# Optimization experiments

Measured on AMD Instinct MI355X. Metric: run time of the kernel, lower is better.

The kernel has to match this reference:

```python
import jax, jax.numpy as jnp
import numpy as np

IN_DIM = 256
OUT_DIM = 256
NUM_HEADS = 4
HEAD_DIM = OUT_DIM // NUM_HEADS
N_SRC = 100000
N_DST = 50000
N_EDGES = 300000


def setup_inputs() -> dict:
    key = jax.random.key(0)
    ks = jax.random.split(key, 10)
    h_src = jax.random.normal(ks[0], (N_SRC, IN_DIM), dtype=jnp.float32)
    h_dst = jax.random.normal(ks[1], (N_DST, IN_DIM), dtype=jnp.float32)
    src_idx = jax.random.randint(ks[2], (N_EDGES,), 0, N_SRC)
    dst_idx = jax.random.randint(ks[3], (N_EDGES,), 0, N_DST)
    # torch nn.Linear weights are [out, in]; xavier-uniform init, zero bias
    def xavier(k, shape):
        limit = jnp.sqrt(6.0 / (shape[0] + shape[1]))
        return jax.random.uniform(k, shape, jnp.float32, -limit, limit)
    Wq = xavier(ks[4], (OUT_DIM, IN_DIM))
    Wk = xavier(ks[5], (OUT_DIM, IN_DIM))
    Wv = xavier(ks[6], (OUT_DIM, IN_DIM))
    bq = jnp.zeros((OUT_DIM,), jnp.float32)
    bk = jnp.zeros((OUT_DIM,), jnp.float32)
    bv = jnp.zeros((OUT_DIM,), jnp.float32)
    return {"h_src": h_src, "h_dst": h_dst, "src_idx": src_idx, "dst_idx": dst_idx,
            "Wq": Wq, "bq": bq, "Wk": Wk, "bk": bk, "Wv": Wv, "bv": bv}


def reference(h_src, h_dst, src_idx, dst_idx, Wq, bq, Wk, bk, Wv, bv):
    # Projections (torch Linear: x @ W.T + b), reshape to [N, H, Dh]
    Q = (h_dst @ Wq.T + bq).reshape(-1, NUM_HEADS, HEAD_DIM)
    K = (h_src @ Wk.T + bk).reshape(-1, NUM_HEADS, HEAD_DIM)
    V = (h_src @ Wv.T + bv).reshape(-1, NUM_HEADS, HEAD_DIM)

    # Edge scores: u_dot_v('K','Q') -> per-edge, per-head dot product [E, H]
    score = jnp.einsum('ehd,ehd->eh', K[src_idx], Q[dst_idx]) / jnp.sqrt(
        jnp.asarray(HEAD_DIM, jnp.float32))

    # Edge softmax grouped by destination (per head), numerically stable
    seg_max = jax.ops.segment_max(score, dst_idx, num_segments=N_DST)
    seg_max = jnp.where(jnp.isfinite(seg_max), seg_max, 0.0)
    e = jnp.exp(score - seg_max[dst_idx])
    seg_sum = jax.ops.segment_sum(e, dst_idx, num_segments=N_DST)
    a = e / seg_sum[dst_idx]  # [E, H]

    # Weighted sum aggregation: u_mul_e then sum per destination
    m = V[src_idx] * a[:, :, None]  # [E, H, Dh]
    h = jax.ops.segment_sum(m, dst_idx, num_segments=N_DST)  # [N_dst, H, Dh]
    return h.reshape(-1, OUT_DIM)
```

## Files before the change

### kernel.cpp

```cpp
#include <hip/hip_runtime.h>
#include <hip/hip_bf16.h>
#include <stdint.h>

#define IN_DIM    256
#define OUT_DIM   256
#define NUM_HEADS 4
#define HEAD_DIM  64
#define N_SRC     100000
#define N_DST     50000
#define N_EDGES   300000

#define BM 128
#define BN 256
#define BK 32
#define SCAN_NBLK ((N_DST + 1023) / 1024)

typedef __attribute__((ext_vector_type(8))) short v8s;
typedef __attribute__((ext_vector_type(4))) float v4f;

__device__ __forceinline__ unsigned short f2bf(float f) {
    unsigned u = __float_as_uint(f);
    unsigned r = (u + 0x7FFFu + ((u >> 16) & 1u)) >> 16;
    return (unsigned short)r;
}
__device__ __forceinline__ float bf2f(unsigned short s) {
    return __uint_as_float(((unsigned)s) << 16);
}

__device__ __forceinline__ void async_copy16(const unsigned short* g,
                                             unsigned short* l) {
    __builtin_amdgcn_global_load_lds(
        (const __attribute__((address_space(1))) unsigned int*)g,
        (__attribute__((address_space(3))) unsigned int*)l, 16, 0, 0);
}

__global__ void wcvt_kernel(const float* __restrict__ wq,
                            const float* __restrict__ wk,
                            const float* __restrict__ wv,
                            unsigned short* __restrict__ dst) {
    int i = blockIdx.x * 256 + threadIdx.x;
    if (i >= 3 * 8192) return;
    int m = i >> 13;
    int r = i & 8191;
    const float* s = (m == 0) ? wq : (m == 1) ? wk : wv;
    const float4* sp = (const float4*)(s + (size_t)r * 8);
    float4 x = sp[0], y = sp[1];
    v8s o;
    o[0] = (short)f2bf(x.x); o[1] = (short)f2bf(x.y);
    o[2] = (short)f2bf(x.z); o[3] = (short)f2bf(x.w);
    o[4] = (short)f2bf(y.x); o[5] = (short)f2bf(y.y);
    o[6] = (short)f2bf(y.z); o[7] = (short)f2bf(y.w);
    *(v8s*)(dst + (size_t)m * 65536 + (size_t)r * 8) = o;
}

__global__ __launch_bounds__(512, 2) void gemm_kernel(
    const float* __restrict__ h_src, const float* __restrict__ h_dst,
    const unsigned short* __restrict__ Wb,
    const float* __restrict__ bq, const float* __restrict__ bk,
    const float* __restrict__ bv,
    unsigned short* __restrict__ Q, unsigned short* __restrict__ K,
    unsigned short* __restrict__ V) {

    __shared__ unsigned short smem[24576];

    int z = blockIdx.z;
    const float* A; const unsigned short* W;
    const float* bias; unsigned short* Out; int M;
    if (z == 0)      { A = h_dst; W = Wb;          bias = bq; Out = Q; M = N_DST; }
    else if (z == 1) { A = h_src; W = Wb + 65536;  bias = bk; Out = K; M = N_SRC; }
    else             { A = h_src; W = Wb + 131072; bias = bv; Out = V; M = N_SRC; }

    int mbase = blockIdx.x * BM;
    if (mbase >= M) return;

    int tid  = threadIdx.x;
    int wave = tid >> 6, lane = tid & 63;
    int lm = lane & 15, quad = lane >> 4;
    int wrow = wave >> 2;
    int wcol = wave & 3;

    int ar = tid >> 2, akc = (tid & 3) * 8;
    int gr = mbase + ar; if (gr > M - 1) gr = M - 1;
    const float* gA = A + (size_t)gr * 256 + akc;

    int sr = lane >> 2, skc = (lane & 3) * 8;
    const unsigned short* gB0 = W + (size_t)(wave * 32 + sr) * 256 + skc;
    const unsigned short* gB1 = gB0 + (size_t)16 * 256;

    v4f acc[4][4];
#pragma unroll
    for (int i = 0; i < 4; i++)
#pragma unroll
        for (int j = 0; j < 4; j++) acc[i][j] = (v4f){0, 0, 0, 0};

    const int NK = 256 / BK;

    float4 xc, yc;
    {
        float4 x0 = *(const float4*)(gA);
        float4 y0 = *(const float4*)(gA + 4);
        async_copy16(gB0, &smem[8192 + (wave * 32) * 32]);
        async_copy16(gB1, &smem[8192 + (wave * 32 + 16) * 32]);
        xc = *(const float4*)(gA + BK);
        yc = *(const float4*)(gA + BK + 4);
        v8s o;
        o[0] = (short)f2bf(x0.x); o[1] = (short)f2bf(x0.y);
        o[2] = (short)f2bf(x0.z); o[3] = (short)f2bf(x0.w);
        o[4] = (short)f2bf(y0.x); o[5] = (short)f2bf(y0.y);
        o[6] = (short)f2bf(y0.z); o[7] = (short)f2bf(y0.w);
        *(v8s*)&smem[(size_t)ar * 32 + akc] = o;
        asm volatile("s_waitcnt vmcnt(2) lgkmcnt(0)" ::: "memory");
        __builtin_amdgcn_s_barrier();
        __builtin_amdgcn_sched_barrier(0);
    }

    int buf = 0;
#pragma unroll
    for (int ks = 0; ks < NK; ks++) {
        float4 xn, yn;
        if (ks + 1 < NK) {
            int k0 = (ks + 1) * BK;
            async_copy16(gB0 + k0,
                         &smem[8192 + (buf ^ 1) * 8192 + (wave * 32) * 32]);
            async_copy16(gB1 + k0,
                         &smem[8192 + (buf ^ 1) * 8192 + (wave * 32 + 16) * 32]);
        }
        if (ks + 2 < NK) {
            int k0 = (ks + 2) * BK;
            xn = *(const float4*)(gA + k0);
            yn = *(const float4*)(gA + k0 + 4);
        }

        const unsigned short* sAb = smem + buf * 4096;
        const unsigned short* sBb = smem + 8192 + buf * 8192;
        v8s af[4], bfr[4];
#pragma unroll
        for (int i = 0; i < 4; i++)
            af[i] = *(const v8s*)&sAb[(wrow * 64 + i * 16 + lm) * 32 + quad * 8];
#pragma unroll
        for (int j = 0; j < 4; j++)
            bfr[j] = *(const v8s*)&sBb[(wcol * 64 + j * 16 + lm) * 32 + quad * 8];
#pragma unroll
        for (int i = 0; i < 4; i++)
#pragma unroll
            for (int j = 0; j < 4; j++)
                acc[i][j] = __builtin_amdgcn_mfma_f32_16x16x32_bf16(
                    af[i], bfr[j], acc[i][j], 0, 0, 0);

        if (ks + 1 < NK) {
            v8s o;
            o[0] = (short)f2bf(xc.x); o[1] = (short)f2bf(xc.y);
            o[2] = (short)f2bf(xc.z); o[3] = (short)f2bf(xc.w);
            o[4] = (short)f2bf(yc.x); o[5] = (short)f2bf(yc.y);
            o[6] = (short)f2bf(yc.z); o[7] = (short)f2bf(yc.w);
            *(v8s*)&smem[(buf ^ 1) * 4096 + (size_t)ar * 32 + akc] = o;
            if (ks + 2 < NK)
                asm volatile("s_waitcnt vmcnt(2) lgkmcnt(0)" ::: "memory");
            else
                asm volatile("s_waitcnt vmcnt(0) lgkmcnt(0)" ::: "memory");
            __builtin_amdgcn_s_barrier();
            __builtin_amdgcn_sched_barrier(0);
        }
        xc = xn; yc = yn;
        buf ^= 1;
    }

#pragma unroll
    for (int p = 0; p < 2; p++) {
        __syncthreads();
        if (wrow == p) {
#pragma unroll
            for (int j = 0; j < 4; j++) {
                int col = wcol * 64 + j * 16 + lm;
                float bcol = bias[col];
#pragma unroll
                for (int i = 0; i < 4; i++)
#pragma unroll
                    for (int r = 0; r < 4; r++)
                        smem[(i * 16 + quad * 4 + r) * 256 + col] =
                            f2bf(acc[i][j][r] + bcol);
            }
        }
        __syncthreads();
#pragma unroll
        for (int k = 0; k < 4; k++) {
            int c = tid + k * 512;
            int rl = c >> 5, ch = c & 31;
            int grow = mbase + p * 64 + rl;
            if (grow < M)
                *(v8s*)(Out + (size_t)grow * 256 + ch * 8) =
                    *(const v8s*)&smem[rl * 256 + ch * 8];
        }
    }
}

__global__ void hist_kernel(const int* __restrict__ dst_idx,
                            int* __restrict__ cnt) {
    int i = blockIdx.x * 256 + threadIdx.x;
    if (i < N_EDGES) atomicAdd(&cnt[dst_idx[i]], 1);
}

__global__ __launch_bounds__(1024) void scan_local_kernel(
    const int* __restrict__ cnt, int* __restrict__ offsets,
    int* __restrict__ bsum) {
    __shared__ int wsum[16];
    int t = threadIdx.x, b = blockIdx.x;
    int i = b * 1024 + t;
    int lane = t & 63, w = t >> 6;
    int v = (i < N_DST) ? cnt[i] : 0;
    int s = v;
#pragma unroll
    for (int off = 1; off < 64; off <<= 1) {
        int u = __shfl_up(s, off, 64);
        if (lane >= off) s += u;
    }
    if (lane == 63) wsum[w] = s;
    __syncthreads();
    if (w == 0) {
        int x = (lane < 16) ? wsum[lane] : 0;
#pragma unroll
        for (int off = 1; off < 16; off <<= 1) {
            int u = __shfl_up(x, off, 64);
            if (lane >= off) x += u;
        }
        if (lane < 16) wsum[lane] = x;
    }
    __syncthreads();
    int wbase = (w == 0) ? 0 : wsum[w - 1];
    if (i < N_DST) offsets[i] = wbase + s - v;
    if (t == 1023) bsum[b] = wsum[15];
}

__global__ void scan_base_kernel(int* __restrict__ bsum,
                                 int* __restrict__ offsets) {
    int lane = threadIdx.x;
    int v = (lane < SCAN_NBLK) ? bsum[lane] : 0;
    int s = v;
#pragma unroll
    for (int off = 1; off < 64; off <<= 1) {
        int u = __shfl_up(s, off, 64);
        if (lane >= off) s += u;
    }
    if (lane < SCAN_NBLK) bsum[lane] = s - v;
    if (lane == 0) offsets[N_DST] = N_EDGES;
}

__global__ __launch_bounds__(1024) void scan_fixup_kernel(
    int* __restrict__ offsets, int* __restrict__ cursor,
    const int* __restrict__ bsum) {
    int i = blockIdx.x * 1024 + threadIdx.x;
    if (i >= N_DST) return;
    int off = offsets[i] + bsum[i >> 10];
    offsets[i] = off;
    cursor[i] = off;
}

__global__ void scatter_kernel(const int* __restrict__ src_idx,
                               const int* __restrict__ dst_idx,
                               int* __restrict__ cursor,
                               int* __restrict__ esrc) {
    int i = blockIdx.x * 256 + threadIdx.x;
    if (i >= N_EDGES) return;
    int d = dst_idx[i];
    int pos = atomicAdd(&cursor[d], 1);
    esrc[pos] = src_idx[i];
}

__global__ __launch_bounds__(256) void agg_kernel(
    const int* __restrict__ esrc, const int* __restrict__ offsets,
    const unsigned short* __restrict__ Q, const unsigned short* __restrict__ K,
    const unsigned short* __restrict__ V, float* __restrict__ out) {

    int wave = threadIdx.x >> 6, lane = threadIdx.x & 63;
    int d = blockIdx.x * 4 + wave;
    if (d >= N_DST) return;

    int start = offsets[d], end = offsets[d + 1];
    float4 o = make_float4(0.f, 0.f, 0.f, 0.f);

    if (end > start) {
        ushort4 qv = *((const ushort4*)(Q + (size_t)d * 256) + lane);
        float q0 = bf2f(qv.x), q1 = bf2f(qv.y), q2 = bf2f(qv.z), q3 = bf2f(qv.w);

        float m = -3.0e38f, l = 0.f;
        float a0 = 0.f, a1 = 0.f, a2 = 0.f, a3 = 0.f;

        int s0 = esrc[start];
        int sN = (start + 1 < end) ? esrc[start + 1] : 0;
        ushort4 kv = *((const ushort4*)(K + (size_t)s0 * 256) + lane);
        ushort4 vv = *((const ushort4*)(V + (size_t)s0 * 256) + lane);

        for (int j = start; j < end; j++) {
            ushort4 kc = kv, vc = vv;
            int sNN = (j + 2 < end) ? esrc[j + 2] : 0;
            if (j + 1 < end) {
                kv = *((const ushort4*)(K + (size_t)sN * 256) + lane);
                vv = *((const ushort4*)(V + (size_t)sN * 256) + lane);
            }
            sN = sNN;

            float p = bf2f(kc.x) * q0 + bf2f(kc.y) * q1 +
                      bf2f(kc.z) * q2 + bf2f(kc.w) * q3;
            p += __shfl_xor(p, 1, 64);
            p += __shfl_xor(p, 2, 64);
            p += __shfl_xor(p, 4, 64);
            p += __shfl_xor(p, 8, 64);
            p *= 0.125f;

            float mn = fmaxf(m, p);
            float sc = __expf(m - mn);
            float w  = __expf(p - mn);
            l = l * sc + w;
            a0 = a0 * sc + w * bf2f(vc.x);
            a1 = a1 * sc + w * bf2f(vc.y);
            a2 = a2 * sc + w * bf2f(vc.z);
            a3 = a3 * sc + w * bf2f(vc.w);
            m = mn;
        }
        float inv = 1.0f / l;
        o = make_float4(a0 * inv, a1 * inv, a2 * inv, a3 * inv);
    }
    *((float4*)(out + (size_t)d * 256) + lane) = o;
}

extern "C" void kernel_launch(void* const* d_in, const int* in_sizes, int n_in,
                              void* d_out, int out_size, void* d_ws, size_t ws_size,
                              hipStream_t stream) {
    const float* h_src   = (const float*)d_in[0];
    const float* h_dst   = (const float*)d_in[1];
    const int*   src_idx = (const int*)d_in[2];
    const int*   dst_idx = (const int*)d_in[3];
    const float* Wq      = (const float*)d_in[4];
    const float* bq      = (const float*)d_in[5];
    const float* Wk      = (const float*)d_in[6];
    const float* bk      = (const float*)d_in[7];
    const float* Wv      = (const float*)d_in[8];
    const float* bv      = (const float*)d_in[9];
    float* out = (float*)d_out;

    char* ws = (char*)d_ws;
    size_t off = 0;
    auto take = [&](size_t bytes) { char* p = ws + off; off = (off + bytes + 255) & ~(size_t)255; return p; };
    unsigned short* Q       = (unsigned short*)take((size_t)N_DST * 256 * 2);
    unsigned short* K       = (unsigned short*)take((size_t)N_SRC * 256 * 2);
    unsigned short* V       = (unsigned short*)take((size_t)N_SRC * 256 * 2);
    unsigned short* Wb      = (unsigned short*)take((size_t)3 * 65536 * 2);
    int*            cnt     = (int*)take((size_t)N_DST * 4);
    int*            offsets = (int*)take((size_t)(N_DST + 1) * 4);
    int*            cursor  = (int*)take((size_t)N_DST * 4);
    int*            esrc    = (int*)take((size_t)N_EDGES * 4);
    int*            bsum    = (int*)take((size_t)64 * 4);
    (void)ws_size; (void)in_sizes; (void)n_in; (void)out_size;

    hipMemsetAsync(cnt, 0, (size_t)N_DST * 4, stream);

    wcvt_kernel<<<96, 256, 0, stream>>>(Wq, Wk, Wv, Wb);

    hist_kernel<<<(N_EDGES + 255) / 256, 256, 0, stream>>>(dst_idx, cnt);
    scan_local_kernel<<<SCAN_NBLK, 1024, 0, stream>>>(cnt, offsets, bsum);
    scan_base_kernel<<<1, 64, 0, stream>>>(bsum, offsets);
    scan_fixup_kernel<<<SCAN_NBLK, 1024, 0, stream>>>(offsets, cursor, bsum);
    scatter_kernel<<<(N_EDGES + 255) / 256, 256, 0, stream>>>(src_idx, dst_idx, cursor, esrc);

    gemm_kernel<<<dim3((N_SRC + BM - 1) / BM, 1, 3), 512, 0, stream>>>(
        h_src, h_dst, Wb, bq, bk, bv, Q, K, V);

    agg_kernel<<<(N_DST + 3) / 4, 256, 0, stream>>>(esrc, offsets, Q, K, V, out);
}
```

Before: 347.0 us.

## Widen GEMM to 1024 threads, fold memset and scan fixup into neighbors

The projection GEMM now runs 16 waves per block, each computing a 64x32 tile instead of 64x64. Each thread stages 4 floats of A and one B row chunk, which halves per-thread accumulators and load work but doubles the wave count. The cnt memset is folded into extra blocks of the weight-convert kernel. The scan fixup kernel is removed by applying the block base offsets lazily in the scatter and aggregation kernels. This cuts kernel launches, but adds more barrier participants and heavier register and occupancy pressure from the requested launch bounds.

After: 359.8 us. 3.7% more time.

```diff
diff --git a/kernel.cpp b/kernel.cpp
--- a/kernel.cpp
+++ b/kernel.cpp
@@ -14,6 +14,7 @@
 #define BN 256
 #define BK 32
 #define SCAN_NBLK ((N_DST + 1023) / 1024)
+#define WCVT_BLKS 96
 
 typedef __attribute__((ext_vector_type(8))) short v8s;
 typedef __attribute__((ext_vector_type(4))) float v4f;
@@ -37,7 +38,13 @@
 __global__ void wcvt_kernel(const float* __restrict__ wq,
                             const float* __restrict__ wk,
                             const float* __restrict__ wv,
-                            unsigned short* __restrict__ dst) {
+                            unsigned short* __restrict__ dst,
+                            int* __restrict__ cnt) {
+    if (blockIdx.x >= WCVT_BLKS) {
+        int i = (blockIdx.x - WCVT_BLKS) * 1024 + threadIdx.x * 4;
+        if (i < N_DST) *(int4*)(cnt + i) = make_int4(0, 0, 0, 0);
+        return;
+    }
     int i = blockIdx.x * 256 + threadIdx.x;
     if (i >= 3 * 8192) return;
     int m = i >> 13;
@@ -53,7 +60,7 @@
     *(v8s*)(dst + (size_t)m * 65536 + (size_t)r * 8) = o;
 }
 
-__global__ __launch_bounds__(512, 2) void gemm_kernel(
+__global__ __launch_bounds__(1024, 5) void gemm_kernel(
     const float* __restrict__ h_src, const float* __restrict__ h_dst,
     const unsigned short* __restrict__ Wb,
     const float* __restrict__ bq, const float* __restrict__ bk,
@@ -76,40 +83,35 @@
     int tid  = threadIdx.x;
     int wave = tid >> 6, lane = tid & 63;
     int lm = lane & 15, quad = lane >> 4;
-    int wrow = wave >> 2;
-    int wcol = wave & 3;
-
-    int ar = tid >> 2, akc = (tid & 3) * 8;
+    int wrow = wave >> 3;
+    int wcol = wave & 7;
+
+    int ar = tid >> 3, akc = (tid & 7) * 4;
     int gr = mbase + ar; if (gr > M - 1) gr = M - 1;
     const float* gA = A + (size_t)gr * 256 + akc;
 
     int sr = lane >> 2, skc = (lane & 3) * 8;
-    const unsigned short* gB0 = W + (size_t)(wave * 32 + sr) * 256 + skc;
-    const unsigned short* gB1 = gB0 + (size_t)16 * 256;
-
-    v4f acc[4][4];
+    const unsigned short* gB0 = W + (size_t)(wave * 16 + sr) * 256 + skc;
+
+    v4f acc[4][2];
 #pragma unroll
     for (int i = 0; i < 4; i++)
 #pragma unroll
-        for (int j = 0; j < 4; j++) acc[i][j] = (v4f){0, 0, 0, 0};
+        for (int j = 0; j < 2; j++) acc[i][j] = (v4f){0, 0, 0, 0};
 
     const int NK = 256 / BK;
 
-    float4 xc, yc;
+    float4 xc;
     {
         float4 x0 = *(const float4*)(gA);
-        float4 y0 = *(const float4*)(gA + 4);
-        async_copy16(gB0, &smem[8192 + (wave * 32) * 32]);
-        async_copy16(gB1, &smem[8192 + (wave * 32 + 16) * 32]);
+        async_copy16(gB0, &smem[8192 + (wave * 16) * 32]);
+        __builtin_amdgcn_sched_barrier(0);
         xc = *(const float4*)(gA + BK);
-        yc = *(const float4*)(gA + BK + 4);
-        v8s o;
-        o[0] = (short)f2bf(x0.x); o[1] = (short)f2bf(x0.y);
-        o[2] = (short)f2bf(x0.z); o[3] = (short)f2bf(x0.w);
-        o[4] = (short)f2bf(y0.x); o[5] = (short)f2bf(y0.y);
-        o[6] = (short)f2bf(y0.z); o[7] = (short)f2bf(y0.w);
-        *(v8s*)&smem[(size_t)ar * 32 + akc] = o;
-        asm volatile("s_waitcnt vmcnt(2) lgkmcnt(0)" ::: "memory");
+        ushort4 o;
+        o.x = f2bf(x0.x); o.y = f2bf(x0.y);
+        o.z = f2bf(x0.z); o.w = f2bf(x0.w);
+        *(ushort4*)&smem[(size_t)ar * 32 + akc] = o;
+        asm volatile("s_waitcnt vmcnt(1) lgkmcnt(0)" ::: "memory");
         __builtin_amdgcn_s_barrier();
         __builtin_amdgcn_sched_barrier(0);
     }
@@ -117,51 +119,47 @@
     int buf = 0;
 #pragma unroll
     for (int ks = 0; ks < NK; ks++) {
-        float4 xn, yn;
+        float4 xn;
         if (ks + 1 < NK) {
-            int k0 = (ks + 1) * BK;
-            async_copy16(gB0 + k0,
-                         &smem[8192 + (buf ^ 1) * 8192 + (wave * 32) * 32]);
-            async_copy16(gB1 + k0,
-                         &smem[8192 + (buf ^ 1) * 8192 + (wave * 32 + 16) * 32]);
-        }
+            async_copy16(gB0 + (ks + 1) * BK,
+                         &smem[8192 + (buf ^ 1) * 8192 + (wave * 16) * 32]);
+        }
+        __builtin_amdgcn_sched_barrier(0);
         if (ks + 2 < NK) {
-            int k0 = (ks + 2) * BK;
-            xn = *(const float4*)(gA + k0);
-            yn = *(const float4*)(gA + k0 + 4);
+            xn = *(const float4*)(gA + (ks + 2) * BK);
         }
 
         const unsigned short* sAb = smem + buf * 4096;
         const unsigned short* sBb = smem + 8192 + buf * 8192;
-        v8s af[4], bfr[4];
+        v8s af[4], bfr[2];
 #pragma unroll
         for (int i = 0; i < 4; i++)
             af[i] = *(const v8s*)&sAb[(wrow * 64 + i * 16 + lm) * 32 + quad * 8];
 #pragma unroll
-        for (int j = 0; j < 4; j++)
-            bfr[j] = *(const v8s*)&sBb[(wcol * 64 + j * 16 + lm) * 32 + quad * 8];
+        for (int j = 0; j < 2; j++)
+            bfr[j] = *(const v8s*)&sBb[(wcol * 32 + j * 16 + lm) * 32 + quad * 8];
 #pragma unroll
         for (int i = 0; i < 4; i++)
 #pragma unroll
-            for (int j = 0; j < 4; j++)
+            for (int j = 0; j < 2; j++)
                 acc[i][j] = __builtin_amdgcn_mfma_f32_16x16x32_bf16(
                     af[i], bfr[j], acc[i][j], 0, 0, 0);
 
         if (ks + 1 < NK) {
-            v8s o;
-            o[0] = (short)f2bf(xc.x); o[1] = (short)f2bf(xc.y);
-            o[2] = (short)f2bf(xc.z); o[3] = (short)f2bf(xc.w);
-            o[4] = (short)f2bf(yc.x); o[5] = (short)f2bf(yc.y);
-            o[6] = (short)f2bf(yc.z); o[7] = (short)f2bf(yc.w);
-            *(v8s*)&smem[(buf ^ 1) * 4096 + (size_t)ar * 32 + akc] = o;
-            if (ks + 2 < NK)
-                asm volatile("s_waitcnt vmcnt(2) lgkmcnt(0)" ::: "memory");
-            else
-                asm volatile("s_waitcnt vmcnt(0) lgkmcnt(0)" ::: "memory");
+            ushort4 o;
+            o.x = f2bf(xc.x); o.y = f2bf(xc.y);
+            o.z = f2bf(xc.z); o.w = f2bf(xc.w);
+            *(ushort4*)&smem[(buf ^ 1) * 4096 + (size_t)ar * 32 + akc] = o;
+        }
+        if (ks <= 5)
+            asm volatile("s_waitcnt vmcnt(1) lgkmcnt(0)" ::: "memory");
+        else if (ks == 6)
+            asm volatile("s_waitcnt vmcnt(0) lgkmcnt(0)" ::: "memory");
+        if (ks < NK - 1) {
             __builtin_amdgcn_s_barrier();
             __builtin_amdgcn_sched_barrier(0);
         }
-        xc = xn; yc = yn;
+        xc = xn;
         buf ^= 1;
     }
 
@@ -170,8 +168,8 @@
         __syncthreads();
         if (wrow == p) {
 #pragma unroll
-            for (int j = 0; j < 4; j++) {
-                int col = wcol * 64 + j * 16 + lm;
+            for (int j = 0; j < 2; j++) {
+                int col = wcol * 32 + j * 16 + lm;
                 float bcol = bias[col];
 #pragma unroll
                 for (int i = 0; i < 4; i++)
@@ -183,8 +181,8 @@
         }
         __syncthreads();
 #pragma unroll
-        for (int k = 0; k < 4; k++) {
-            int c = tid + k * 512;
+        for (int k = 0; k < 2; k++) {
+            int c = tid + k * 1024;
             int rl = c >> 5, ch = c & 31;
             int grow = mbase + p * 64 + rl;
             if (grow < M)
@@ -202,7 +200,7 @@
 
 __global__ __launch_bounds__(1024) void scan_local_kernel(
     const int* __restrict__ cnt, int* __restrict__ offsets,
-    int* __restrict__ bsum) {
+    int* __restrict__ cursor, int* __restrict__ bsum) {
     __shared__ int wsum[16];
     int t = threadIdx.x, b = blockIdx.x;
     int i = b * 1024 + t;
@@ -227,12 +225,15 @@
     }
     __syncthreads();
     int wbase = (w == 0) ? 0 : wsum[w - 1];
-    if (i < N_DST) offsets[i] = wbase + s - v;
+    if (i < N_DST) {
+        int e = wbase + s - v;
+        offsets[i] = e;
+        cursor[i] = e;
+    }
     if (t == 1023) bsum[b] = wsum[15];
 }
 
-__global__ void scan_base_kernel(int* __restrict__ bsum,
-                                 int* __restrict__ offsets) {
+__global__ void scan_base_kernel(int* __restrict__ bsum) {
     int lane = threadIdx.x;
     int v = (lane < SCAN_NBLK) ? bsum[lane] : 0;
     int s = v;
@@ -242,32 +243,23 @@
         if (lane >= off) s += u;
     }
     if (lane < SCAN_NBLK) bsum[lane] = s - v;
-    if (lane == 0) offsets[N_DST] = N_EDGES;
-}
-
-__global__ __launch_bounds__(1024) void scan_fixup_kernel(
-    int* __restrict__ offsets, int* __restrict__ cursor,
-    const int* __restrict__ bsum) {
-    int i = blockIdx.x * 1024 + threadIdx.x;
-    if (i >= N_DST) return;
-    int off = offsets[i] + bsum[i >> 10];
-    offsets[i] = off;
-    cursor[i] = off;
 }
 
 __global__ void scatter_kernel(const int* __restrict__ src_idx,
                                const int* __restrict__ dst_idx,
                                int* __restrict__ cursor,
+                               const int* __restrict__ bsum,
                                int* __restrict__ esrc) {
     int i = blockIdx.x * 256 + threadIdx.x;
     if (i >= N_EDGES) return;
     int d = dst_idx[i];
-    int pos = atomicAdd(&cursor[d], 1);
+    int pos = atomicAdd(&cursor[d], 1) + bsum[d >> 10];
     esrc[pos] = src_idx[i];
 }
 
 __global__ __launch_bounds__(256) void agg_kernel(
     const int* __restrict__ esrc, const int* __restrict__ offsets,
+    const int* __restrict__ bsum,
     const unsigned short* __restrict__ Q, const unsigned short* __restrict__ K,
     const unsigned short* __restrict__ V, float* __restrict__ out) {
 
@@ -275,7 +267,9 @@
     int d = blockIdx.x * 4 + wave;
     if (d >= N_DST) return;
 
-    int start = offsets[d], end = offsets[d + 1];
+    int start = offsets[d] + bsum[d >> 10];
+    int end = (d + 1 == N_DST) ? N_EDGES
+                               : offsets[d + 1] + bsum[(d + 1) >> 10];
     float4 o = make_float4(0.f, 0.f, 0.f, 0.f);
 
     if (end > start) {
@@ -352,18 +346,16 @@
     int*            bsum    = (int*)take((size_t)64 * 4);
     (void)ws_size; (void)in_sizes; (void)n_in; (void)out_size;
 
-    hipMemsetAsync(cnt, 0, (size_t)N_DST * 4, stream);
-
-    wcvt_kernel<<<96, 256, 0, stream>>>(Wq, Wk, Wv, Wb);
+    wcvt_kernel<<<WCVT_BLKS + SCAN_NBLK, 256, 0, stream>>>(Wq, Wk, Wv, Wb, cnt);
 
     hist_kernel<<<(N_EDGES + 255) / 256, 256, 0, stream>>>(dst_idx, cnt);
-    scan_local_kernel<<<SCAN_NBLK, 1024, 0, stream>>>(cnt, offsets, bsum);
-    scan_base_kernel<<<1, 64, 0, stream>>>(bsum, offsets);
-    scan_fixup_kernel<<<SCAN_NBLK, 1024, 0, stream>>>(offsets, cursor, bsum);
-    scatter_kernel<<<(N_EDGES + 255) / 256, 256, 0, stream>>>(src_idx, dst_idx, cursor, esrc);
-
-    gemm_kernel<<<dim3((N_SRC + BM - 1) / BM, 1, 3), 512, 0, stream>>>(
+    scan_local_kernel<<<SCAN_NBLK, 1024, 0, stream>>>(cnt, offsets, cursor, bsum);
+    scan_base_kernel<<<1, 64, 0, stream>>>(bsum);
+    scatter_kernel<<<(N_EDGES + 255) / 256, 256, 0, stream>>>(src_idx, dst_idx,
+                                                              cursor, bsum, esrc);
+
+    gemm_kernel<<<dim3((N_SRC + BM - 1) / BM, 1, 3), 1024, 0, stream>>>(
         h_src, h_dst, Wb, bq, bk, bv, Q, K, V);
 
-    agg_kernel<<<(N_DST + 3) / 4, 256, 0, stream>>>(esrc, offsets, Q, K, V, out);
-}
+    agg_kernel<<<(N_DST + 3) / 4, 256, 0, stream>>>(esrc, offsets, bsum, Q, K, V, out);
+}
```
